# Optimization experiments

Measured on AMD Instinct MI355X. Metric: run time of the kernel, lower is better.

## Reference

```python
import jax, jax.numpy as jnp
import numpy as np

V = 32000   # vocab_size
HD = 512    # num_hiddens
B = 32      # batch
T = 128     # seq_len


def setup_inputs() -> dict:
    key = jax.random.key(0)
    ks = jax.random.split(key, 11)
    s_in = 1.0 / np.sqrt(V + HD)   # torch Linear default init bound
    s_out = 1.0 / np.sqrt(HD)

    def lin_w(k, out_f, in_f, s):
        return jax.random.uniform(k, (out_f, in_f), jnp.float32, -s, s)

    def lin_b(k, out_f, s):
        return jax.random.uniform(k, (out_f,), jnp.float32, -s, s)

    return {
        "X": jax.random.randint(ks[0], (B, T), 0, V),
        "H": jnp.zeros((B, HD), jnp.float32),
        "C": jnp.zeros((B, HD), jnp.float32),
        "Wf": lin_w(ks[1], HD, V + HD, s_in), "bf": lin_b(ks[2], HD, s_in),
        "Wi": lin_w(ks[3], HD, V + HD, s_in), "bi": lin_b(ks[4], HD, s_in),
        "Wo": lin_w(ks[5], HD, V + HD, s_in), "bo": lin_b(ks[6], HD, s_in),
        "Wc": lin_w(ks[7], HD, V + HD, s_in), "bc": lin_b(ks[8], HD, s_in),
        "Wy": lin_w(ks[9], V, HD, s_out),     "by": lin_b(ks[10], V, s_out),
    }


def reference(X, H, C, Wf, bf, Wi, bi, Wo, bo, Wc, bc, Wy, by):
    # X: [B, T] int tokens. Transposed to time-major like torch's X.T.
    Xt = X.T  # [T, B]
    hd = H.shape[1]
    v = Wf.shape[1] - hd

    def split(W):
        return W[:, :v], W[:, v:]  # input part, hidden part

    Wfx, Wfh = split(Wf)
    Wix, Wih = split(Wi)
    Wox, Woh = split(Wo)
    Wcx, Wch = split(Wc)

    # one_hot(x) @ Wx^T == row-gather of Wx^T: same math, no wasted compute.
    Ef = jnp.take(Wfx.T, Xt, axis=0) + bf  # [T, B, HD]
    Ei = jnp.take(Wix.T, Xt, axis=0) + bi
    Eo = jnp.take(Wox.T, Xt, axis=0) + bo
    Ec = jnp.take(Wcx.T, Xt, axis=0) + bc

    def step(carry, e):
        h, c = carry
        ef, ei, eo, ec = e
        f = jax.nn.sigmoid(ef + h @ Wfh.T)
        i = jax.nn.sigmoid(ei + h @ Wih.T)
        o = jax.nn.sigmoid(eo + h @ Woh.T)
        c_tilde = jnp.tanh(ec + h @ Wch.T)
        c = f * c + i * c_tilde
        h = o * jnp.tanh(c)
        return (h, c), h

    (H, C), Hs = jax.lax.scan(step, (H, C), (Ef, Ei, Eo, Ec))  # Hs: [T, B, HD]

    # per-step Y = h2out(H), then torch.cat(outputs, dim=0) -> [T*B, V]
    Y = Hs.reshape(-1, hd) @ Wy.T + by
    return Y, (H, C)
```

## Files before the change

### kernel.cpp

```cpp
#include <hip/hip_runtime.h>
#include <hip/hip_bf16.h>

#define V  32000
#define HD 512
#define BB 32
#define TT 128
#define VH 32512
#define LBLK 8
#define NBLK 256
#define NGEMM (NBLK - LBLK - 1)
#define NTILE (32 * 125)

typedef short  short8  __attribute__((ext_vector_type(8)));
typedef unsigned short u16x8 __attribute__((ext_vector_type(8)));
typedef unsigned short u16x4 __attribute__((ext_vector_type(4)));
typedef float  f32x4   __attribute__((ext_vector_type(4)));

__device__ __forceinline__ unsigned short bf16_rne(float f) {
  unsigned u = __builtin_bit_cast(unsigned, f);
  u += 0x7FFFu + ((u >> 16) & 1u);
  return (unsigned short)(u >> 16);
}

__device__ __forceinline__ void gload_lds16(const void* g, void* l) {
  __builtin_amdgcn_global_load_lds((const __attribute__((address_space(1))) void*)g,
                                   (__attribute__((address_space(3))) void*)l, 16, 0, 0);
}

__device__ __forceinline__ float sigf(float x) {
  return 1.0f / (1.0f + __expf(-x));
}
__device__ __forceinline__ float tanhf_fast(float x) {
  return 1.0f - 2.0f / (1.0f + __expf(2.0f * x));
}

__device__ __forceinline__ unsigned aload(const unsigned* p) {
  return __hip_atomic_load(p, __ATOMIC_RELAXED, __HIP_MEMORY_SCOPE_AGENT);
}
__device__ __forceinline__ void astore(unsigned* p, unsigned v) {
  __hip_atomic_store(p, v, __ATOMIC_RELAXED, __HIP_MEMORY_SCOPE_AGENT);
}
__device__ __forceinline__ unsigned aadd(unsigned* p, unsigned v) {
  return __hip_atomic_fetch_add(p, v, __ATOMIC_RELAXED, __HIP_MEMORY_SCOPE_AGENT);
}

__device__ __forceinline__ void run_tiles(
    char* smem, const unsigned short* Hs, const unsigned short* Wyb,
    const float* by, float* Y, unsigned* bar2, unsigned* tcount)
{
  const int tid = threadIdx.x;
  const int wid = tid >> 6, lane = tid & 63;
  const int fr = lane & 15, ko = lane >> 4;
  const int wr = wid >> 2, wc = wid & 3;
  unsigned short* As = (unsigned short*)smem;
  unsigned short* Bs = (unsigned short*)(smem + 16384);
  int* sh_tile = (int*)(smem + 49216);

  while (true) {
    if (tid == 0) *sh_tile = (int)aadd(tcount, 1u);
    __syncthreads();
    const int tile = *sh_tile;
    if (tile >= NTILE) break;
    const int bm = tile / 125, bn = tile % 125;
    const int row0 = bm << 7, col0 = bn << 8;

    if (tid == 0) {
      const unsigned need = (unsigned)(4 * bm + 4);
      while (aload(bar2) < need)
        __builtin_amdgcn_s_sleep(32);
    }
    __syncthreads();

    f32x4 acc[4][4];
    #pragma unroll
    for (int m = 0; m < 4; ++m)
      #pragma unroll
      for (int n = 0; n < 4; ++n)
        acc[m][n] = (f32x4){0.f, 0.f, 0.f, 0.f};

    for (int kt = 0; kt < 8; ++kt) {
      const int k0 = kt << 6;
      #pragma unroll
      for (int is = 0; is < 2; ++is) {
        const int id = is * 512 + tid;
        const int r = id >> 3;
        const int c = (id & 7) ^ (r & 7);
        gload_lds16(Hs + (size_t)(row0 + r) * 512 + k0 + c * 8,
                    &As[(is * 512 + (tid & ~63)) * 8]);
      }
      #pragma unroll
      for (int is = 0; is < 4; ++is) {
        const int id = is * 512 + tid;
        const int r = id >> 3;
        const int c = (id & 7) ^ (r & 7);
        gload_lds16(Wyb + (size_t)(col0 + r) * 512 + k0 + c * 8,
                    &Bs[(is * 512 + (tid & ~63)) * 8]);
      }
      __syncthreads();
      #pragma unroll
      for (int kk = 0; kk < 2; ++kk) {
        short8 af[4], bfr[4];
        #pragma unroll
        for (int m = 0; m < 4; ++m) {
          const int r = (wr << 6) + (m << 4) + fr;
          const int c = ((kk << 2) | ko) ^ (r & 7);
          af[m] = *(const short8*)&As[r * 64 + c * 8];
        }
        #pragma unroll
        for (int n = 0; n < 4; ++n) {
          const int r = (wc << 6) + (n << 4) + fr;
          const int c = ((kk << 2) | ko) ^ (r & 7);
          bfr[n] = *(const short8*)&Bs[r * 64 + c * 8];
        }
        #pragma unroll
        for (int m = 0; m < 4; ++m)
          #pragma unroll
          for (int n = 0; n < 4; ++n)
            acc[m][n] = __builtin_amdgcn_mfma_f32_16x16x32_bf16(
                af[m], bfr[n], acc[m][n], 0, 0, 0);
      }
      __syncthreads();
    }

    const int rgrp = lane >> 4;
    #pragma unroll
    for (int n = 0; n < 4; ++n) {
      const int col = col0 + (wc << 6) + (n << 4) + fr;
      const float bias = by[col];
      #pragma unroll
      for (int m = 0; m < 4; ++m) {
        const int rowb = row0 + (wr << 6) + (m << 4) + (rgrp << 2);
        #pragma unroll
        for (int j = 0; j < 4; ++j) {
          __builtin_nontemporal_store(acc[m][n][j] + bias,
                                      &Y[(size_t)(rowb + j) * V + col]);
        }
      }
    }
  }
}

__global__ void __launch_bounds__(512, 2) fused_all(
    const int* __restrict__ X,
    const float* __restrict__ Hin,
    const float* __restrict__ Cin,
    const float* __restrict__ Wf, const float* __restrict__ bfp,
    const float* __restrict__ Wi, const float* __restrict__ bip,
    const float* __restrict__ Wo, const float* __restrict__ bop,
    const float* __restrict__ Wc, const float* __restrict__ bcp,
    const float* __restrict__ Wy, const float* __restrict__ by,
    float* __restrict__ E,
    unsigned short* __restrict__ HsM1,
    unsigned short* __restrict__ Wyb,
    float* __restrict__ outHC,
    unsigned* __restrict__ bar2,
    unsigned* __restrict__ wbar,
    unsigned* __restrict__ tcount,
    unsigned* __restrict__ eflag,
    unsigned* __restrict__ wflag,
    unsigned* __restrict__ lticket,
    unsigned* __restrict__ gticket,
    float* __restrict__ Y)
{
  __shared__ __align__(16) char smem[75776];
  __shared__ int sh_role, sh_x0;

  const int tid = threadIdx.x;
  const int wid = tid >> 6, lane = tid & 63;
  const int fr = lane & 15, ko = lane >> 4;
  const int rowgrp = lane >> 4;

  unsigned short* Hs = HsM1 + BB * HD;

  if (tid == 0) {
    unsigned xcd;
    asm volatile("s_getreg_b32 %0, hwreg(20, 0, 32)" : "=s"(xcd));
    int role = -1;
    if (xcd == 0) {
      const unsigned s = aadd(lticket, 1u);
      if (s < (unsigned)LBLK) role = (int)s;
      else if (s == (unsigned)LBLK) role = 100;
    }
    if (role == -1) {
      const unsigned g = aadd(gticket, 1u);
      role = -(int)g - 2;
    }
    sh_role = role;
    sh_x0 = (xcd == 0) ? 1 : 0;
  }
  __syncthreads();
  const int role = sh_role;

  if (role >= 0 && role < LBLK) {
    short* hl = (short*)smem;

    const int blk = role;
    const int qb = blk * 64 + wid * 8;
    unsigned* myflag = &wflag[(blk * 8 + wid) * 16];

    short8 wreg[2][16];
    #pragma unroll
    for (int mt = 0; mt < 2; ++mt) {
      const int qA = qb + mt * 4 + (fr >> 2);
      const int gA = fr & 3;
      const float* WgA = (gA == 0) ? Wf : (gA == 1) ? Wi : (gA == 2) ? Wo : Wc;
      const float* rowp = WgA + (size_t)qA * VH + V;
      #pragma unroll
      for (int kk = 0; kk < 16; ++kk) {
        const float4 lo = *(const float4*)(rowp + kk * 32 + ko * 8);
        const float4 hi = *(const float4*)(rowp + kk * 32 + ko * 8 + 4);
        short8 w;
        w[0] = (short)bf16_rne(lo.x); w[1] = (short)bf16_rne(lo.y);
        w[2] = (short)bf16_rne(lo.z); w[3] = (short)bf16_rne(lo.w);
        w[4] = (short)bf16_rne(hi.x); w[5] = (short)bf16_rne(hi.y);
        w[6] = (short)bf16_rne(hi.z); w[7] = (short)bf16_rne(hi.w);
        wreg[mt][kk] = w;
      }
    }

    float creg[2][2];
    #pragma unroll
    for (int mt = 0; mt < 2; ++mt)
      #pragma unroll
      for (int nt = 0; nt < 2; ++nt) {
        const int b = nt * 16 + fr;
        const int q = qb + mt * 4 + rowgrp;
        creg[mt][nt] = Cin[b * HD + q];
        HsM1[(size_t)b * HD + q] = bf16_rne(Hin[b * HD + q]);
      }
    asm volatile("s_waitcnt vmcnt(0)" ::: "memory");
    if (lane == 0) astore(myflag, 1u);

    while (aload(&eflag[0]) < 4u) {}
    f32x4 eldc[2][2];
    {
      const float* Eb0 = E;
      #pragma unroll
      for (int mt = 0; mt < 2; ++mt)
        #pragma unroll
        for (int nt = 0; nt < 2; ++nt) {
          const int b = nt * 16 + fr;
          const int q = qb + mt * 4 + rowgrp;
          eldc[mt][nt] = *(const f32x4*)(Eb0 + ((size_t)b * HD + q) * 4);
        }
    }

    const int bsw = (fr & 7) << 4;
    const int bbase0 = fr * 1024;
    const int bbase1 = (16 + fr) * 1024;

    for (int t = 0; t < TT; ++t) {
      {
        const unsigned* pa = &wflag[lane * 16];
        const unsigned need = (unsigned)(t + 1);
        const bool echk = (lane == 0) && (t + 1 < TT);
        while (true) {
          bool ok = aload(pa) >= need;
          if (echk) ok = ok && (aload(&eflag[t + 1]) >= 4u);
          if (__all((int)ok)) break;
        }
      }

      const char* hsrc = (const char*)(HsM1 + (size_t)t * (BB * HD));
      #pragma unroll
      for (int is = 0; is < 4; ++is) {
        const int i = is * 512 + tid;
        const int sb = (i >> 6) * 1024 + (((i & 63) * 16) ^ (((i >> 6) & 7) << 4));
        gload_lds16(hsrc + sb, (char*)hl + (size_t)(is * 512 + (tid & ~63)) * 16);
      }
      __syncthreads();

      f32x4 eldn[2][2];
      if (t + 1 < TT) {
        const float* Ebn = E + (size_t)(t + 1) * BB * HD * 4;
        #pragma unroll
        for (int mt = 0; mt < 2; ++mt)
          #pragma unroll
          for (int nt = 0; nt < 2; ++nt) {
            const int b = nt * 16 + fr;
            const int q = qb + mt * 4 + rowgrp;
            eldn[mt][nt] = *(const f32x4*)(Ebn + ((size_t)b * HD + q) * 4);
          }
      }

      f32x4 acc[2][2];
      #pragma unroll
      for (int mt = 0; mt < 2; ++mt)
        #pragma unroll
        for (int nt = 0; nt < 2; ++nt)
          acc[mt][nt] = (f32x4){0.f, 0.f, 0.f, 0.f};
      #pragma unroll
      for (int kk = 0; kk < 16; ++kk) {
        const int off = kk * 64 + ko * 16;
        const short8 b0 = *(const short8*)((const char*)hl + bbase0 + (off ^ bsw));
        const short8 b1 = *(const short8*)((const char*)hl + bbase1 + (off ^ bsw));
        acc[0][0] = __builtin_amdgcn_mfma_f32_16x16x32_bf16(wreg[0][kk], b0, acc[0][0], 0, 0, 0);
        acc[0][1] = __builtin_amdgcn_mfma_f32_16x16x32_bf16(wreg[0][kk], b1, acc[0][1], 0, 0, 0);
        acc[1][0] = __builtin_amdgcn_mfma_f32_16x16x32_bf16(wreg[1][kk], b0, acc[1][0], 0, 0, 0);
        acc[1][1] = __builtin_amdgcn_mfma_f32_16x16x32_bf16(wreg[1][kk], b1, acc[1][1], 0, 0, 0);
      }

      unsigned short* hstore = HsM1 + (size_t)(t + 1) * (BB * HD);
      #pragma unroll
      for (int mt = 0; mt < 2; ++mt)
        #pragma unroll
        for (int nt = 0; nt < 2; ++nt) {
          const int b = nt * 16 + fr;
          const int q = qb + mt * 4 + rowgrp;
          const f32x4 a = acc[mt][nt];
          const f32x4 e4 = eldc[mt][nt];
          const float fg = sigf(a[0] + e4[0]);
          const float ig = sigf(a[1] + e4[1]);
          const float og = sigf(a[2] + e4[2]);
          const float ct = tanhf_fast(a[3] + e4[3]);
          const float cn = fg * creg[mt][nt] + ig * ct;
          const float hv = og * tanhf_fast(cn);
          creg[mt][nt] = cn;
          hstore[(size_t)b * HD + q] = bf16_rne(hv);
          if (t == TT - 1) {
            outHC[(size_t)b * HD + q] = hv;
            outHC[(size_t)BB * HD + b * HD + q] = cn;
          }
        }

      asm volatile("s_waitcnt vmcnt(0)" ::: "memory");
      if (lane == 0) astore(myflag, (unsigned)(t + 2));

      #pragma unroll
      for (int mt = 0; mt < 2; ++mt)
        #pragma unroll
        for (int nt = 0; nt < 2; ++nt)
          eldc[mt][nt] = eldn[mt][nt];
    }

    while (aload(wbar) < (unsigned)NGEMM)
      __builtin_amdgcn_s_sleep(8);
    __syncthreads();
    run_tiles(smem, Hs, Wyb, by, Y, bar2, tcount);

  } else if (role == 100) {
    if (wid == 0) {
      for (int T = 8; T <= TT; T += 8) {
        const unsigned need = (unsigned)(T + 1);
        while (true) {
          const unsigned v = aload(&wflag[lane * 16]);
          if (__all((int)(v >= need))) break;
          __builtin_amdgcn_s_sleep(2);
        }
        if (lane == 0) {
          __threadfence();
          astore(bar2, (unsigned)T);
        }
      }
    }
    __syncthreads();
    while (aload(wbar) < (unsigned)NGEMM)
      __builtin_amdgcn_s_sleep(8);
    __syncthreads();
    run_tiles(smem, Hs, Wyb, by, Y, bar2, tcount);

  } else {
    int* xs = (int*)(smem + 49152);
    const int gid = -role - 2;
    const int x0 = sh_x0;

    for (int u = gid; u < 4 * TT; u += NGEMM) {
      const int tg = u >> 2, qtr = u & 3;
      if (tid < 8) xs[tid] = X[(qtr * 8 + tid) * TT + tg];
      __syncthreads();
      const int q = tid;
      const float b0v = bfp[q], b1v = bip[q], b2v = bop[q], b3v = bcp[q];
      float* Ebase = E + (size_t)tg * BB * HD * 4;
      #pragma unroll
      for (int b = 0; b < 8; ++b) {
        const int xv = xs[b];
        f32x4 ev;
        ev[0] = __builtin_nontemporal_load(Wf + (size_t)q * VH + xv) + b0v;
        ev[1] = __builtin_nontemporal_load(Wi + (size_t)q * VH + xv) + b1v;
        ev[2] = __builtin_nontemporal_load(Wo + (size_t)q * VH + xv) + b2v;
        ev[3] = __builtin_nontemporal_load(Wc + (size_t)q * VH + xv) + b3v;
        __builtin_nontemporal_store(ev,
            (f32x4*)(Ebase + ((size_t)(qtr * 8 + b) * HD + q) * 4));
      }
      __syncthreads();
      if (tid == 0) {
        __threadfence();
        aadd(&eflag[tg], 1u);
      }
    }

    {
      const size_t n = (size_t)V * HD;
      for (size_t i = ((size_t)gid * 512 + tid) * 8; i < n;
           i += (size_t)NGEMM * 512 * 8) {
        const f32x4 a = __builtin_nontemporal_load((const f32x4*)(Wy + i));
        const f32x4 b = __builtin_nontemporal_load((const f32x4*)(Wy + i + 4));
        u16x8 o;
        o[0] = bf16_rne(a[0]); o[1] = bf16_rne(a[1]); o[2] = bf16_rne(a[2]); o[3] = bf16_rne(a[3]);
        o[4] = bf16_rne(b[0]); o[5] = bf16_rne(b[1]); o[6] = bf16_rne(b[2]); o[7] = bf16_rne(b[3]);
        *(u16x8*)(Wyb + i) = o;
      }
      __syncthreads();
      if (tid == 0) {
        __threadfence();
        aadd(wbar, 1u);
        while (aload(wbar) < (unsigned)NGEMM)
          __builtin_amdgcn_s_sleep(2);
      }
      __syncthreads();
    }

    if (x0) {
      if (tid == 0) {
        while (aload(bar2) < (unsigned)TT)
          __builtin_amdgcn_s_sleep(64);
      }
      __syncthreads();
    }

    run_tiles(smem, Hs, Wyb, by, Y, bar2, tcount);
  }
}

extern "C" void kernel_launch(void* const* d_in, const int* in_sizes, int n_in,
                              void* d_out, int out_size, void* d_ws, size_t ws_size,
                              hipStream_t stream)
{
  const int*   X  = (const int*)  d_in[0];
  const float* H  = (const float*)d_in[1];
  const float* C  = (const float*)d_in[2];
  const float* Wf = (const float*)d_in[3];
  const float* bf = (const float*)d_in[4];
  const float* Wi = (const float*)d_in[5];
  const float* bi = (const float*)d_in[6];
  const float* Wo = (const float*)d_in[7];
  const float* bo = (const float*)d_in[8];
  const float* Wc = (const float*)d_in[9];
  const float* bc = (const float*)d_in[10];
  const float* Wy = (const float*)d_in[11];
  const float* by = (const float*)d_in[12];

  float* Y = (float*)d_out;
  float* outHC = Y + (size_t)TT * BB * V;

  char* ws = (char*)d_ws;
  float* E              = (float*)ws;
  unsigned short* Wyb   = (unsigned short*)(ws + 33554432);
  unsigned short* HsM1  = (unsigned short*)(ws + 66322432);
  char* ctrl            = ws + 70549504;
  unsigned* lticket     = (unsigned*)(ctrl + 0);
  unsigned* gticket     = (unsigned*)(ctrl + 64);
  unsigned* bar2        = (unsigned*)(ctrl + 128);
  unsigned* wbar        = (unsigned*)(ctrl + 192);
  unsigned* tcount      = (unsigned*)(ctrl + 256);
  unsigned* eflag       = (unsigned*)(ctrl + 320);
  unsigned* wflag       = (unsigned*)(ctrl + 1024);

  (void)hipMemsetAsync(ctrl, 0, 6144, stream);

  {
    const int* X_p = X;
    const float *H_p = H, *C_p = C;
    const float *Wf_p = Wf, *bf_p = bf, *Wi_p = Wi, *bi_p = bi;
    const float *Wo_p = Wo, *bo_p = bo, *Wc_p = Wc, *bc_p = bc;
    const float *Wy_p = Wy, *by_p = by;
    float* E_p = E;
    unsigned short* HsM1_p = HsM1;
    unsigned short* Wyb_p = Wyb;
    float* outHC_p = outHC;
    unsigned *bar2_p = bar2, *wbar_p = wbar, *tcount_p = tcount;
    unsigned *eflag_p = eflag, *wflag_p = wflag;
    unsigned *lticket_p = lticket, *gticket_p = gticket;
    float* Y_p = Y;
    void* args[] = {(void*)&X_p, (void*)&H_p, (void*)&C_p,
                    (void*)&Wf_p, (void*)&bf_p, (void*)&Wi_p, (void*)&bi_p,
                    (void*)&Wo_p, (void*)&bo_p, (void*)&Wc_p, (void*)&bc_p,
                    (void*)&Wy_p, (void*)&by_p,
                    (void*)&E_p, (void*)&HsM1_p, (void*)&Wyb_p, (void*)&outHC_p,
                    (void*)&bar2_p, (void*)&wbar_p, (void*)&tcount_p,
                    (void*)&eflag_p, (void*)&wflag_p,
                    (void*)&lticket_p, (void*)&gticket_p,
                    (void*)&Y_p};
    (void)hipLaunchCooperativeKernel((void*)fused_all, dim3(NBLK), dim3(512), args, 0, stream);
  }
}
```

Baseline: 866.8 us.

## Split LSTM recurrence into two independent batch halves with separate flags

The recurrent step is split into two batch halves (rows 0-15 and 16-31), each with its own global readiness flag array. One half can load its H slice, run MFMAs and publish its flag while the other half is still waiting on slower blocks, which shortens the critical path of the cross-block barrier. The cost is two syncs per step instead of one, extra flag traffic, and a larger memset.

Result: slower. 1.066 ms (+23.0%).

```diff
diff --git a/kernel.cpp b/kernel.cpp
--- a/kernel.cpp
+++ b/kernel.cpp
@@ -157,7 +157,8 @@
     unsigned* __restrict__ wbar,
     unsigned* __restrict__ tcount,
     unsigned* __restrict__ eflag,
-    unsigned* __restrict__ wflag,
+    unsigned* __restrict__ wflagA,
+    unsigned* __restrict__ wflagB,
     unsigned* __restrict__ lticket,
     unsigned* __restrict__ gticket,
     float* __restrict__ Y)
@@ -196,7 +197,8 @@
 
     const int blk = role;
     const int qb = blk * 64 + wid * 8;
-    unsigned* myflag = &wflag[(blk * 8 + wid) * 16];
+    unsigned* myflagA = &wflagA[(blk * 8 + wid) * 16];
+    unsigned* myflagB = &wflagB[(blk * 8 + wid) * 16];
 
     short8 wreg[2][16];
     #pragma unroll
@@ -229,7 +231,7 @@
         HsM1[(size_t)b * HD + q] = bf16_rne(Hin[b * HD + q]);
       }
     asm volatile("s_waitcnt vmcnt(0)" ::: "memory");
-    if (lane == 0) astore(myflag, 1u);
+    if (lane == 0) { astore(myflagA, 1u); astore(myflagB, 1u); }
 
     while (aload(&eflag[0]) < 4u) {}
     f32x4 eldc[2][2];
@@ -250,87 +252,124 @@
     const int bbase1 = (16 + fr) * 1024;
 
     for (int t = 0; t < TT; ++t) {
+      unsigned short* hstore = HsM1 + (size_t)(t + 1) * (BB * HD);
+      const char* hsrc = (const char*)(HsM1 + (size_t)t * (BB * HD));
+      const float* Ebn = E + (size_t)(t + 1) * BB * HD * 4;
+
       {
-        const unsigned* pa = &wflag[lane * 16];
         const unsigned need = (unsigned)(t + 1);
         const bool echk = (lane == 0) && (t + 1 < TT);
         while (true) {
-          bool ok = aload(pa) >= need;
+          bool ok = aload(&wflagA[lane * 16]) >= need;
           if (echk) ok = ok && (aload(&eflag[t + 1]) >= 4u);
           if (__all((int)ok)) break;
         }
       }
-
-      const char* hsrc = (const char*)(HsM1 + (size_t)t * (BB * HD));
-      #pragma unroll
-      for (int is = 0; is < 4; ++is) {
+      #pragma unroll
+      for (int is = 0; is < 2; ++is) {
         const int i = is * 512 + tid;
         const int sb = (i >> 6) * 1024 + (((i & 63) * 16) ^ (((i >> 6) & 7) << 4));
         gload_lds16(hsrc + sb, (char*)hl + (size_t)(is * 512 + (tid & ~63)) * 16);
       }
       __syncthreads();
 
-      f32x4 eldn[2][2];
-      if (t + 1 < TT) {
-        const float* Ebn = E + (size_t)(t + 1) * BB * HD * 4;
-        #pragma unroll
-        for (int mt = 0; mt < 2; ++mt)
-          #pragma unroll
-          for (int nt = 0; nt < 2; ++nt) {
-            const int b = nt * 16 + fr;
-            const int q = qb + mt * 4 + rowgrp;
-            eldn[mt][nt] = *(const f32x4*)(Ebn + ((size_t)b * HD + q) * 4);
-          }
-      }
-
-      f32x4 acc[2][2];
-      #pragma unroll
-      for (int mt = 0; mt < 2; ++mt)
-        #pragma unroll
-        for (int nt = 0; nt < 2; ++nt)
-          acc[mt][nt] = (f32x4){0.f, 0.f, 0.f, 0.f};
-      #pragma unroll
-      for (int kk = 0; kk < 16; ++kk) {
-        const int off = kk * 64 + ko * 16;
-        const short8 b0 = *(const short8*)((const char*)hl + bbase0 + (off ^ bsw));
-        const short8 b1 = *(const short8*)((const char*)hl + bbase1 + (off ^ bsw));
-        acc[0][0] = __builtin_amdgcn_mfma_f32_16x16x32_bf16(wreg[0][kk], b0, acc[0][0], 0, 0, 0);
-        acc[0][1] = __builtin_amdgcn_mfma_f32_16x16x32_bf16(wreg[0][kk], b1, acc[0][1], 0, 0, 0);
-        acc[1][0] = __builtin_amdgcn_mfma_f32_16x16x32_bf16(wreg[1][kk], b0, acc[1][0], 0, 0, 0);
-        acc[1][1] = __builtin_amdgcn_mfma_f32_16x16x32_bf16(wreg[1][kk], b1, acc[1][1], 0, 0, 0);
-      }
-
-      unsigned short* hstore = HsM1 + (size_t)(t + 1) * (BB * HD);
-      #pragma unroll
-      for (int mt = 0; mt < 2; ++mt)
-        #pragma unroll
-        for (int nt = 0; nt < 2; ++nt) {
-          const int b = nt * 16 + fr;
+      {
+        f32x4 a0 = (f32x4){0.f, 0.f, 0.f, 0.f};
+        f32x4 a1 = (f32x4){0.f, 0.f, 0.f, 0.f};
+        #pragma unroll
+        for (int kk = 0; kk < 16; ++kk) {
+          const int off = kk * 64 + ko * 16;
+          const short8 b0 = *(const short8*)((const char*)hl + bbase0 + (off ^ bsw));
+          a0 = __builtin_amdgcn_mfma_f32_16x16x32_bf16(wreg[0][kk], b0, a0, 0, 0, 0);
+          a1 = __builtin_amdgcn_mfma_f32_16x16x32_bf16(wreg[1][kk], b0, a1, 0, 0, 0);
+        }
+        #pragma unroll
+        for (int mt = 0; mt < 2; ++mt) {
+          const int b = fr;
           const int q = qb + mt * 4 + rowgrp;
-          const f32x4 a = acc[mt][nt];
-          const f32x4 e4 = eldc[mt][nt];
+          const f32x4 a = (mt == 0) ? a0 : a1;
+          const f32x4 e4 = eldc[mt][0];
           const float fg = sigf(a[0] + e4[0]);
           const float ig = sigf(a[1] + e4[1]);
           const float og = sigf(a[2] + e4[2]);
           const float ct = tanhf_fast(a[3] + e4[3]);
-          const float cn = fg * creg[mt][nt] + ig * ct;
+          const float cn = fg * creg[mt][0] + ig * ct;
           const float hv = og * tanhf_fast(cn);
-          creg[mt][nt] = cn;
+          creg[mt][0] = cn;
           hstore[(size_t)b * HD + q] = bf16_rne(hv);
           if (t == TT - 1) {
             outHC[(size_t)b * HD + q] = hv;
             outHC[(size_t)BB * HD + b * HD + q] = cn;
           }
         }
-
+      }
       asm volatile("s_waitcnt vmcnt(0)" ::: "memory");
-      if (lane == 0) astore(myflag, (unsigned)(t + 2));
-
-      #pragma unroll
-      for (int mt = 0; mt < 2; ++mt)
-        #pragma unroll
-        for (int nt = 0; nt < 2; ++nt)
-          eldc[mt][nt] = eldn[mt][nt];
+      if (lane == 0) astore(myflagA, (unsigned)(t + 2));
+      if (t + 1 < TT) {
+        #pragma unroll
+        for (int mt = 0; mt < 2; ++mt) {
+          const int b = fr;
+          const int q = qb + mt * 4 + rowgrp;
+          eldc[mt][0] = *(const f32x4*)(Ebn + ((size_t)b * HD + q) * 4);
+        }
+      }
+
+      {
+        const unsigned need = (unsigned)(t + 1);
+        while (true) {
+          const unsigned v = aload(&wflagB[lane * 16]);
+          if (__all((int)(v >= need))) break;
+        }
+      }
+      #pragma unroll
+      for (int is = 0; is < 2; ++is) {
+        const int i = 1024 + is * 512 + tid;
+        const int sb = (i >> 6) * 1024 + (((i & 63) * 16) ^ (((i >> 6) & 7) << 4));
+        gload_lds16(hsrc + sb,
+                    (char*)hl + (size_t)(1024 + is * 512 + (tid & ~63)) * 16);
+      }
+      __syncthreads();
+
+      {
+        f32x4 a0 = (f32x4){0.f, 0.f, 0.f, 0.f};
+        f32x4 a1 = (f32x4){0.f, 0.f, 0.f, 0.f};
+        #pragma unroll
+        for (int kk = 0; kk < 16; ++kk) {
+          const int off = kk * 64 + ko * 16;
+          const short8 b1 = *(const short8*)((const char*)hl + bbase1 + (off ^ bsw));
+          a0 = __builtin_amdgcn_mfma_f32_16x16x32_bf16(wreg[0][kk], b1, a0, 0, 0, 0);
+          a1 = __builtin_amdgcn_mfma_f32_16x16x32_bf16(wreg[1][kk], b1, a1, 0, 0, 0);
+        }
+        #pragma unroll
+        for (int mt = 0; mt < 2; ++mt) {
+          const int b = 16 + fr;
+          const int q = qb + mt * 4 + rowgrp;
+          const f32x4 a = (mt == 0) ? a0 : a1;
+          const f32x4 e4 = eldc[mt][1];
+          const float fg = sigf(a[0] + e4[0]);
+          const float ig = sigf(a[1] + e4[1]);
+          const float og = sigf(a[2] + e4[2]);
+          const float ct = tanhf_fast(a[3] + e4[3]);
+          const float cn = fg * creg[mt][1] + ig * ct;
+          const float hv = og * tanhf_fast(cn);
+          creg[mt][1] = cn;
+          hstore[(size_t)b * HD + q] = bf16_rne(hv);
+          if (t == TT - 1) {
+            outHC[(size_t)b * HD + q] = hv;
+            outHC[(size_t)BB * HD + b * HD + q] = cn;
+          }
+        }
+      }
+      asm volatile("s_waitcnt vmcnt(0)" ::: "memory");
+      if (lane == 0) astore(myflagB, (unsigned)(t + 2));
+      if (t + 1 < TT) {
+        #pragma unroll
+        for (int mt = 0; mt < 2; ++mt) {
+          const int b = 16 + fr;
+          const int q = qb + mt * 4 + rowgrp;
+          eldc[mt][1] = *(const f32x4*)(Ebn + ((size_t)b * HD + q) * 4);
+        }
+      }
     }
 
     while (aload(wbar) < (unsigned)NGEMM)
@@ -343,8 +382,9 @@
       for (int T = 8; T <= TT; T += 8) {
         const unsigned need = (unsigned)(T + 1);
         while (true) {
-          const unsigned v = aload(&wflag[lane * 16]);
-          if (__all((int)(v >= need))) break;
+          const unsigned va = aload(&wflagA[lane * 16]);
+          const unsigned vb = aload(&wflagB[lane * 16]);
+          if (__all((int)(va >= need && vb >= need))) break;
           __builtin_amdgcn_s_sleep(2);
         }
         if (lane == 0) {
@@ -454,9 +494,10 @@
   unsigned* wbar        = (unsigned*)(ctrl + 192);
   unsigned* tcount      = (unsigned*)(ctrl + 256);
   unsigned* eflag       = (unsigned*)(ctrl + 320);
-  unsigned* wflag       = (unsigned*)(ctrl + 1024);
-
-  (void)hipMemsetAsync(ctrl, 0, 6144, stream);
+  unsigned* wflagA      = (unsigned*)(ctrl + 1024);
+  unsigned* wflagB      = (unsigned*)(ctrl + 5120);
+
+  (void)hipMemsetAsync(ctrl, 0, 16384, stream);
 
   {
     const int* X_p = X;
@@ -469,7 +510,7 @@
     unsigned short* Wyb_p = Wyb;
     float* outHC_p = outHC;
     unsigned *bar2_p = bar2, *wbar_p = wbar, *tcount_p = tcount;
-    unsigned *eflag_p = eflag, *wflag_p = wflag;
+    unsigned *eflag_p = eflag, *wflagA_p = wflagA, *wflagB_p = wflagB;
     unsigned *lticket_p = lticket, *gticket_p = gticket;
     float* Y_p = Y;
     void* args[] = {(void*)&X_p, (void*)&H_p, (void*)&C_p,
@@ -478,7 +519,7 @@
                     (void*)&Wy_p, (void*)&by_p,
                     (void*)&E_p, (void*)&HsM1_p, (void*)&Wyb_p, (void*)&outHC_p,
                     (void*)&bar2_p, (void*)&wbar_p, (void*)&tcount_p,
-                    (void*)&eflag_p, (void*)&wflag_p,
+                    (void*)&eflag_p, (void*)&wflagA_p, (void*)&wflagB_p,
                     (void*)&lticket_p, (void*)&gticket_p,
                     (void*)&Y_p};
     (void)hipLaunchCooperativeKernel((void*)fused_all, dim3(NBLK), dim3(512), args, 0, stream);
```
